# Kernel optimization log

Measured on AMD Instinct MI355X. Metric: run time of the kernel, lower is better.

## Reference

```python
import jax, jax.numpy as jnp
import numpy as np

P = 16  # patch size
D = 768  # embedding dim


def setup_inputs() -> dict:
    key = jax.random.key(0)
    k_img, k_w, k_b = jax.random.split(key, 3)
    B, H, W, C = 64, 224, 224, 3
    image = jax.random.normal(k_img, (B, H, W, C), dtype=jnp.float32)
    patch_dim = P * P * C  # 768
    # Keras Dense default: glorot_uniform kernel, zeros bias
    limit = np.sqrt(6.0 / (patch_dim + D)).astype(np.float32)
    W_proj = jax.random.uniform(k_w, (patch_dim, D), dtype=jnp.float32,
                                minval=-limit, maxval=limit)
    b_proj = jnp.zeros((D,), dtype=jnp.float32)
    return {"image": image, "W_proj": W_proj, "b_proj": b_proj}


def reference(image, W_proj, b_proj):
    B, H, W, C = image.shape
    nh, nw = H // P, W // P
    # Fused im2col replacing the per-patch slicing loop:
    # [B,H,W,C] -> [B, nh, P, nw, P, C] -> [B, nh, nw, P, P, C] -> [B, nh*nw, P*P*C]
    # Row-major (p_i, p_j) patch order matches the original nested loop, and
    # flatten of a [B,P,P,C] slice matches the (P,P,C) raveling here.
    patches = image.reshape(B, nh, P, nw, P, C)
    patches = patches.transpose(0, 1, 3, 2, 4, 5).reshape(B, nh * nw, P * P * C)
    # Dense + exact GELU (tf.keras.activations.gelu default approximate=False)
    x = jnp.einsum('bnp,pd->bnd', patches, W_proj) + b_proj
    return jax.nn.gelu(x, approximate=False)
```

## Files before the change

### kernel.cpp

```cpp
#include <hip/hip_runtime.h>
#include <hip/hip_bf16.h>
#include <math.h>

#define MM 12544
#define KK 768
#define NN 768
#define BM 64
#define BN 256
#define NKS 24
#define MT 196
#define NT 3
#define N64 12

#define A2_BLOCKS (MT * 4)
#define W_BLOCKS (N64 * NKS)
#define FRAG_BYTES 1024
#define KSTRIDE (4 * FRAG_BYTES)
#define PANEL_BYTES (NKS * KSTRIDE)

typedef __bf16 v8bf __attribute__((ext_vector_type(8)));
typedef float  v4f  __attribute__((ext_vector_type(4)));

__global__ __launch_bounds__(256) void pack_kernel(const float* __restrict__ img,
                                                   const float* __restrict__ w,
                                                   __hip_bfloat16* __restrict__ apack,
                                                   __hip_bfloat16* __restrict__ wpack) {
    const int tid = threadIdx.x;

    if (blockIdx.x < A2_BLOCKS) {
        const int blk = blockIdx.x;
        const int mt  = blk >> 2;
        const int c   = blk & 3;
        const int r   = tid & 63;
        const int il  = tid >> 6;
        const int i   = c * 4 + il;
        const int m   = mt * 64 + r;
        const int b   = m / 196;
        const int pm  = m - b * 196;
        const int pr  = pm / 14;
        const int pc  = pm - pr * 14;
        const float* src = img + (size_t)(((b * 224 + pr * 16 + i) * 224 + pc * 16) * 3);
        float4 f[12];
#pragma unroll
        for (int ld = 0; ld < 12; ld++) f[ld] = ((const float4*)src)[ld];

        const int fi   = r >> 4;
        const int l_lo = r & 15;
        uint4* dst = (uint4*)apack + ((size_t)(mt * 24) * 4 + fi) * 64 + l_lo;
#pragma unroll
        for (int j = 0; j < 6; j++) {
            const int G  = i * 6 + j;
            const int ks = G >> 2;
            const int lh = G & 3;
            union { __hip_bfloat16 hh[8]; uint4 uu; } o;
            o.hh[0] = __float2bfloat16(f[2*j].x);   o.hh[1] = __float2bfloat16(f[2*j].y);
            o.hh[2] = __float2bfloat16(f[2*j].z);   o.hh[3] = __float2bfloat16(f[2*j].w);
            o.hh[4] = __float2bfloat16(f[2*j+1].x); o.hh[5] = __float2bfloat16(f[2*j+1].y);
            o.hh[6] = __float2bfloat16(f[2*j+1].z); o.hh[7] = __float2bfloat16(f[2*j+1].w);
            dst[(size_t)ks * 256 + lh * 16] = o.uu;
        }
    } else {
        const int bid = blockIdx.x - A2_BLOCKS;
        const int gid = bid * 256 + tid;
        const int l    = gid & 63;
        const int fi   = (gid >> 6) & 3;
        const int wb   = gid >> 8;
        const int n64  = wb / NKS;
        const int ks   = wb - n64 * NKS;
        const int col  = n64 * 64 + fi * 16 + (l & 15);
        const int k0   = ks * 32 + (l >> 4) * 8;
        union { __hip_bfloat16 hh[8]; uint4 uu; } o;
#pragma unroll
        for (int j = 0; j < 8; j++) o.hh[j] = __float2bfloat16(w[(size_t)(k0 + j) * NN + col]);
        ((uint4*)wpack)[(size_t)((n64 * NKS + ks) * 4 + fi) * 64 + l] = o.uu;
    }
}

__device__ __forceinline__ float gelu_fast(float x) {
    float t2 = 1.5957691216057308f * x * (1.0f + 0.044715f * x * x);
    float e  = __expf(t2);
    float r  = __builtin_amdgcn_rcpf(e + 1.0f);
    return x - x * r;
}

__global__ __launch_bounds__(256, 3) void gemm_reg(const __hip_bfloat16* __restrict__ apack,
                                                   const __hip_bfloat16* __restrict__ wpack,
                                                   const float* __restrict__ bias,
                                                   float* __restrict__ out) {
    const int h   = blockIdx.x;
    const int xcd = h & 7;
    const int jj  = h >> 3;
    const int u   = (xcd < 4 ? xcd * 74 : 296 + (xcd - 4) * 73) + jj;
    const int nt  = u % 3;
    const int mt  = u / 3;

    const int tid  = threadIdx.x;
    const int lane = tid & 63;
    const int wave = tid >> 6;
    const int col  = lane & 15;
    const int quad = lane >> 4;

    const char* pA = (const char*)apack + (size_t)mt * PANEL_BYTES + lane * 16;
    const char* pB = (const char*)wpack + (size_t)(nt * 4 + wave) * PANEL_BYTES + lane * 16;

    v4f acc[4][4];
    const v4f vzero = {0.f, 0.f, 0.f, 0.f};
#pragma unroll
    for (int a = 0; a < 4; a++)
#pragma unroll
        for (int c = 0; c < 4; c++) acc[a][c] = vzero;

    v8bf aR[2][4], bR[2][4];
#pragma unroll
    for (int mi = 0; mi < 4; mi++) {
        aR[0][mi] = *(const v8bf*)(pA + mi * FRAG_BYTES);
        aR[1][mi] = *(const v8bf*)(pA + KSTRIDE + mi * FRAG_BYTES);
    }
#pragma unroll
    for (int ni = 0; ni < 4; ni++) {
        bR[0][ni] = *(const v8bf*)(pB + ni * FRAG_BYTES);
        bR[1][ni] = *(const v8bf*)(pB + KSTRIDE + ni * FRAG_BYTES);
    }

#pragma unroll
    for (int ks = 0; ks < NKS; ks++) {
        const int cur = ks & 1;
        __builtin_amdgcn_s_setprio(1);
#pragma unroll
        for (int mi = 0; mi < 4; mi++)
#pragma unroll
            for (int ni = 0; ni < 4; ni++)
                acc[mi][ni] = __builtin_amdgcn_mfma_f32_16x16x32_bf16(
                    aR[cur][mi], bR[cur][ni], acc[mi][ni], 0, 0, 0);
        __builtin_amdgcn_s_setprio(0);
        if (ks + 2 < NKS) {
            const char* qA = pA + (size_t)(ks + 2) * KSTRIDE;
            const char* qB = pB + (size_t)(ks + 2) * KSTRIDE;
#pragma unroll
            for (int mi = 0; mi < 4; mi++)
                aR[cur][mi] = *(const v8bf*)(qA + mi * FRAG_BYTES);
#pragma unroll
            for (int ni = 0; ni < 4; ni++)
                bR[cur][ni] = *(const v8bf*)(qB + ni * FRAG_BYTES);
        }
    }

#pragma unroll
    for (int ni = 0; ni < 4; ni++) {
        int n    = nt * BN + wave * 64 + ni * 16 + col;
        float bv = bias[n];
#pragma unroll
        for (int mi = 0; mi < 4; mi++) {
            int rowb = mt * BM + mi * 16 + quad * 4;
            float* po = out + (size_t)rowb * NN + n;
#pragma unroll
            for (int rg = 0; rg < 4; rg++) {
                float x = acc[mi][ni][rg] + bv;
                po[(size_t)rg * NN] = gelu_fast(x);
            }
        }
    }
}

extern "C" void kernel_launch(void* const* d_in, const int* in_sizes, int n_in,
                              void* d_out, int out_size, void* d_ws, size_t ws_size,
                              hipStream_t stream) {
    const float* img   = (const float*)d_in[0];
    const float* wproj = (const float*)d_in[1];
    const float* bias  = (const float*)d_in[2];
    float* out = (float*)d_out;

    __hip_bfloat16* apack = (__hip_bfloat16*)d_ws;
    __hip_bfloat16* wpack = (__hip_bfloat16*)((char*)d_ws + (size_t)MM * KK * 2);

    pack_kernel<<<dim3(A2_BLOCKS + W_BLOCKS), dim3(256), 0, stream>>>(
        img, wproj, apack, wpack);
    gemm_reg<<<dim3(MT * NT), dim3(256), 0, stream>>>(apack, wpack, bias, out);
}
```

Measured before the change: 120.5 us.

## Fuse pack and GEMM into one persistent kernel with atomic work queue

Replaces the separate pack and GEMM launches with a single persistent kernel of 768 blocks. Blocks pull items from an atomic queue: weight packing first, then image packing, then GEMM tiles. Each GEMM tile spin-waits on completion counters for the weight pack and for its own A panel. This removes the gap between the two launches and lets GEMM work overlap with packing, at the cost of a memset, atomic traffic and spin-wait stalls, plus a deadlock risk if ordering assumptions fail.

```diff
diff --git a/kernel.cpp b/kernel.cpp
--- a/kernel.cpp
+++ b/kernel.cpp
@@ -12,69 +12,23 @@
 #define NT 3
 #define N64 12
 
-#define A2_BLOCKS (MT * 4)
-#define W_BLOCKS (N64 * NKS)
+#define W_ITEMS 288
+#define A_ITEMS (MT * 4)
+#define PACK_ITEMS (W_ITEMS + A_ITEMS)
+#define G_ITEMS (MT * NT)
+#define TOTAL_ITEMS (PACK_ITEMS + G_ITEMS)
+#define NBLK_PERS 768
+
 #define FRAG_BYTES 1024
 #define KSTRIDE (4 * FRAG_BYTES)
 #define PANEL_BYTES (NKS * KSTRIDE)
 
+#define APACK_BYTES ((size_t)MM * KK * 2)
+#define WPACK_BYTES ((size_t)NN * KK * 2)
+#define CTRS_OFF (APACK_BYTES + WPACK_BYTES)
+
 typedef __bf16 v8bf __attribute__((ext_vector_type(8)));
 typedef float  v4f  __attribute__((ext_vector_type(4)));
-
-__global__ __launch_bounds__(256) void pack_kernel(const float* __restrict__ img,
-                                                   const float* __restrict__ w,
-                                                   __hip_bfloat16* __restrict__ apack,
-                                                   __hip_bfloat16* __restrict__ wpack) {
-    const int tid = threadIdx.x;
-
-    if (blockIdx.x < A2_BLOCKS) {
-        const int blk = blockIdx.x;
-        const int mt  = blk >> 2;
-        const int c   = blk & 3;
-        const int r   = tid & 63;
-        const int il  = tid >> 6;
-        const int i   = c * 4 + il;
-        const int m   = mt * 64 + r;
-        const int b   = m / 196;
-        const int pm  = m - b * 196;
-        const int pr  = pm / 14;
-        const int pc  = pm - pr * 14;
-        const float* src = img + (size_t)(((b * 224 + pr * 16 + i) * 224 + pc * 16) * 3);
-        float4 f[12];
-#pragma unroll
-        for (int ld = 0; ld < 12; ld++) f[ld] = ((const float4*)src)[ld];
-
-        const int fi   = r >> 4;
-        const int l_lo = r & 15;
-        uint4* dst = (uint4*)apack + ((size_t)(mt * 24) * 4 + fi) * 64 + l_lo;
-#pragma unroll
-        for (int j = 0; j < 6; j++) {
-            const int G  = i * 6 + j;
-            const int ks = G >> 2;
-            const int lh = G & 3;
-            union { __hip_bfloat16 hh[8]; uint4 uu; } o;
-            o.hh[0] = __float2bfloat16(f[2*j].x);   o.hh[1] = __float2bfloat16(f[2*j].y);
-            o.hh[2] = __float2bfloat16(f[2*j].z);   o.hh[3] = __float2bfloat16(f[2*j].w);
-            o.hh[4] = __float2bfloat16(f[2*j+1].x); o.hh[5] = __float2bfloat16(f[2*j+1].y);
-            o.hh[6] = __float2bfloat16(f[2*j+1].z); o.hh[7] = __float2bfloat16(f[2*j+1].w);
-            dst[(size_t)ks * 256 + lh * 16] = o.uu;
-        }
-    } else {
-        const int bid = blockIdx.x - A2_BLOCKS;
-        const int gid = bid * 256 + tid;
-        const int l    = gid & 63;
-        const int fi   = (gid >> 6) & 3;
-        const int wb   = gid >> 8;
-        const int n64  = wb / NKS;
-        const int ks   = wb - n64 * NKS;
-        const int col  = n64 * 64 + fi * 16 + (l & 15);
-        const int k0   = ks * 32 + (l >> 4) * 8;
-        union { __hip_bfloat16 hh[8]; uint4 uu; } o;
-#pragma unroll
-        for (int j = 0; j < 8; j++) o.hh[j] = __float2bfloat16(w[(size_t)(k0 + j) * NN + col]);
-        ((uint4*)wpack)[(size_t)((n64 * NKS + ks) * 4 + fi) * 64 + l] = o.uu;
-    }
-}
 
 __device__ __forceinline__ float gelu_fast(float x) {
     float t2 = 1.5957691216057308f * x * (1.0f + 0.044715f * x * x);
@@ -83,82 +37,161 @@
     return x - x * r;
 }
 
-__global__ __launch_bounds__(256, 3) void gemm_reg(const __hip_bfloat16* __restrict__ apack,
-                                                   const __hip_bfloat16* __restrict__ wpack,
-                                                   const float* __restrict__ bias,
-                                                   float* __restrict__ out) {
-    const int h   = blockIdx.x;
-    const int xcd = h & 7;
-    const int jj  = h >> 3;
-    const int u   = (xcd < 4 ? xcd * 74 : 296 + (xcd - 4) * 73) + jj;
-    const int nt  = u % 3;
-    const int mt  = u / 3;
-
-    const int tid  = threadIdx.x;
-    const int lane = tid & 63;
-    const int wave = tid >> 6;
-    const int col  = lane & 15;
-    const int quad = lane >> 4;
-
-    const char* pA = (const char*)apack + (size_t)mt * PANEL_BYTES + lane * 16;
-    const char* pB = (const char*)wpack + (size_t)(nt * 4 + wave) * PANEL_BYTES + lane * 16;
-
-    v4f acc[4][4];
-    const v4f vzero = {0.f, 0.f, 0.f, 0.f};
-#pragma unroll
-    for (int a = 0; a < 4; a++)
-#pragma unroll
-        for (int c = 0; c < 4; c++) acc[a][c] = vzero;
-
-    v8bf aR[2][4], bR[2][4];
-#pragma unroll
-    for (int mi = 0; mi < 4; mi++) {
-        aR[0][mi] = *(const v8bf*)(pA + mi * FRAG_BYTES);
-        aR[1][mi] = *(const v8bf*)(pA + KSTRIDE + mi * FRAG_BYTES);
-    }
-#pragma unroll
-    for (int ni = 0; ni < 4; ni++) {
-        bR[0][ni] = *(const v8bf*)(pB + ni * FRAG_BYTES);
-        bR[1][ni] = *(const v8bf*)(pB + KSTRIDE + ni * FRAG_BYTES);
-    }
-
-#pragma unroll
-    for (int ks = 0; ks < NKS; ks++) {
-        const int cur = ks & 1;
-        __builtin_amdgcn_s_setprio(1);
-#pragma unroll
-        for (int mi = 0; mi < 4; mi++)
-#pragma unroll
-            for (int ni = 0; ni < 4; ni++)
-                acc[mi][ni] = __builtin_amdgcn_mfma_f32_16x16x32_bf16(
-                    aR[cur][mi], bR[cur][ni], acc[mi][ni], 0, 0, 0);
-        __builtin_amdgcn_s_setprio(0);
-        if (ks + 2 < NKS) {
-            const char* qA = pA + (size_t)(ks + 2) * KSTRIDE;
-            const char* qB = pB + (size_t)(ks + 2) * KSTRIDE;
-#pragma unroll
-            for (int mi = 0; mi < 4; mi++)
-                aR[cur][mi] = *(const v8bf*)(qA + mi * FRAG_BYTES);
-#pragma unroll
-            for (int ni = 0; ni < 4; ni++)
-                bR[cur][ni] = *(const v8bf*)(qB + ni * FRAG_BYTES);
+__global__ __launch_bounds__(256, 3) void fused_all(const float* __restrict__ img,
+                                                    const float* __restrict__ w,
+                                                    const float* __restrict__ bias,
+                                                    float* __restrict__ out,
+                                                    __hip_bfloat16* __restrict__ apack,
+                                                    __hip_bfloat16* __restrict__ wpack,
+                                                    unsigned int* __restrict__ ctrs) {
+    unsigned int* queue = ctrs;
+    unsigned int* wdone = ctrs + 1;
+    unsigned int* adone = ctrs + 2;
+
+    __shared__ int s_item;
+    const int tid = threadIdx.x;
+
+    int it = blockIdx.x;
+    for (;;) {
+        if (it >= TOTAL_ITEMS) break;
+        unsigned int* fptr = nullptr;
+
+        if (it < W_ITEMS) {
+            const int l   = tid & 63;
+            const int fi  = tid >> 6;
+            const int n64 = it / NKS;
+            const int ks  = it - n64 * NKS;
+            const int col = n64 * 64 + fi * 16 + (l & 15);
+            const int k0  = ks * 32 + (l >> 4) * 8;
+            union { __hip_bfloat16 hh[8]; uint4 uu; } o;
+#pragma unroll
+            for (int j = 0; j < 8; j++)
+                o.hh[j] = __float2bfloat16(w[(size_t)(k0 + j) * NN + col]);
+            ((uint4*)wpack)[(size_t)((n64 * NKS + ks) * 4 + fi) * 64 + l] = o.uu;
+            fptr = wdone;
+        } else if (it < PACK_ITEMS) {
+            const int a   = it - W_ITEMS;
+            const int mt  = a >> 2;
+            const int c   = a & 3;
+            const int r   = tid & 63;
+            const int il  = tid >> 6;
+            const int i   = c * 4 + il;
+            const int m   = mt * 64 + r;
+            const int b   = m / 196;
+            const int pm  = m - b * 196;
+            const int pr  = pm / 14;
+            const int pc  = pm - pr * 14;
+            const float* src = img + (size_t)(((b * 224 + pr * 16 + i) * 224 + pc * 16) * 3);
+            float4 f[12];
+#pragma unroll
+            for (int ld = 0; ld < 12; ld++) f[ld] = ((const float4*)src)[ld];
+            const int fi   = r >> 4;
+            const int l_lo = r & 15;
+            uint4* dst = (uint4*)apack + ((size_t)(mt * 24) * 4 + fi) * 64 + l_lo;
+#pragma unroll
+            for (int j = 0; j < 6; j++) {
+                const int G  = i * 6 + j;
+                const int ks = G >> 2;
+                const int lh = G & 3;
+                union { __hip_bfloat16 hh[8]; uint4 uu; } o;
+                o.hh[0] = __float2bfloat16(f[2*j].x);   o.hh[1] = __float2bfloat16(f[2*j].y);
+                o.hh[2] = __float2bfloat16(f[2*j].z);   o.hh[3] = __float2bfloat16(f[2*j].w);
+                o.hh[4] = __float2bfloat16(f[2*j+1].x); o.hh[5] = __float2bfloat16(f[2*j+1].y);
+                o.hh[6] = __float2bfloat16(f[2*j+1].z); o.hh[7] = __float2bfloat16(f[2*j+1].w);
+                dst[(size_t)ks * 256 + lh * 16] = o.uu;
+            }
+            fptr = &adone[mt];
+        } else {
+            const int g  = it - PACK_ITEMS;
+            const int mt = g / 3;
+            const int nt = g - mt * 3;
+
+            if (tid == 0) {
+                while (__hip_atomic_load(wdone, __ATOMIC_RELAXED,
+                                         __HIP_MEMORY_SCOPE_AGENT) < W_ITEMS)
+                    __builtin_amdgcn_s_sleep(2);
+                while (__hip_atomic_load(&adone[mt], __ATOMIC_RELAXED,
+                                         __HIP_MEMORY_SCOPE_AGENT) < 4)
+                    __builtin_amdgcn_s_sleep(2);
+            }
+            __syncthreads();
+            __threadfence();
+
+            const int lane = tid & 63;
+            const int wave = tid >> 6;
+            const int col  = lane & 15;
+            const int quad = lane >> 4;
+
+            const char* pA = (const char*)apack + (size_t)mt * PANEL_BYTES + lane * 16;
+            const char* pB = (const char*)wpack + (size_t)(nt * 4 + wave) * PANEL_BYTES + lane * 16;
+
+            v4f acc[4][4];
+            const v4f vzero = {0.f, 0.f, 0.f, 0.f};
+#pragma unroll
+            for (int aa = 0; aa < 4; aa++)
+#pragma unroll
+                for (int cc = 0; cc < 4; cc++) acc[aa][cc] = vzero;
+
+            v8bf aR[2][4], bR[2][4];
+#pragma unroll
+            for (int mi = 0; mi < 4; mi++) {
+                aR[0][mi] = *(const v8bf*)(pA + mi * FRAG_BYTES);
+                aR[1][mi] = *(const v8bf*)(pA + KSTRIDE + mi * FRAG_BYTES);
+            }
+#pragma unroll
+            for (int ni = 0; ni < 4; ni++) {
+                bR[0][ni] = *(const v8bf*)(pB + ni * FRAG_BYTES);
+                bR[1][ni] = *(const v8bf*)(pB + KSTRIDE + ni * FRAG_BYTES);
+            }
+#pragma unroll
+            for (int ks = 0; ks < NKS; ks++) {
+                const int cur = ks & 1;
+                __builtin_amdgcn_s_setprio(1);
+#pragma unroll
+                for (int mi = 0; mi < 4; mi++)
+#pragma unroll
+                    for (int ni = 0; ni < 4; ni++)
+                        acc[mi][ni] = __builtin_amdgcn_mfma_f32_16x16x32_bf16(
+                            aR[cur][mi], bR[cur][ni], acc[mi][ni], 0, 0, 0);
+                __builtin_amdgcn_s_setprio(0);
+                if (ks + 2 < NKS) {
+                    const char* qA = pA + (size_t)(ks + 2) * KSTRIDE;
+                    const char* qB = pB + (size_t)(ks + 2) * KSTRIDE;
+#pragma unroll
+                    for (int mi = 0; mi < 4; mi++)
+                        aR[cur][mi] = *(const v8bf*)(qA + mi * FRAG_BYTES);
+#pragma unroll
+                    for (int ni = 0; ni < 4; ni++)
+                        bR[cur][ni] = *(const v8bf*)(qB + ni * FRAG_BYTES);
+                }
+            }
+#pragma unroll
+            for (int ni = 0; ni < 4; ni++) {
+                int n    = nt * BN + wave * 64 + ni * 16 + col;
+                float bv = bias[n];
+#pragma unroll
+                for (int mi = 0; mi < 4; mi++) {
+                    int rowb = mt * BM + mi * 16 + quad * 4;
+                    float* po = out + (size_t)rowb * NN + n;
+#pragma unroll
+                    for (int rg = 0; rg < 4; rg++) {
+                        float x = acc[mi][ni][rg] + bv;
+                        po[(size_t)rg * NN] = gelu_fast(x);
+                    }
+                }
+            }
         }
-    }
-
-#pragma unroll
-    for (int ni = 0; ni < 4; ni++) {
-        int n    = nt * BN + wave * 64 + ni * 16 + col;
-        float bv = bias[n];
-#pragma unroll
-        for (int mi = 0; mi < 4; mi++) {
-            int rowb = mt * BM + mi * 16 + quad * 4;
-            float* po = out + (size_t)rowb * NN + n;
-#pragma unroll
-            for (int rg = 0; rg < 4; rg++) {
-                float x = acc[mi][ni][rg] + bv;
-                po[(size_t)rg * NN] = gelu_fast(x);
-            }
+
+        __syncthreads();
+        if (tid == 0) {
+            if (fptr) {
+                __threadfence();
+                atomicAdd(fptr, 1u);
+            }
+            s_item = NBLK_PERS + (int)atomicAdd(queue, 1u);
         }
+        __syncthreads();
+        it = s_item;
     }
 }
 
@@ -171,9 +204,10 @@
     float* out = (float*)d_out;
 
     __hip_bfloat16* apack = (__hip_bfloat16*)d_ws;
-    __hip_bfloat16* wpack = (__hip_bfloat16*)((char*)d_ws + (size_t)MM * KK * 2);
-
-    pack_kernel<<<dim3(A2_BLOCKS + W_BLOCKS), dim3(256), 0, stream>>>(
-        img, wproj, apack, wpack);
-    gemm_reg<<<dim3(MT * NT), dim3(256), 0, stream>>>(apack, wpack, bias, out);
+    __hip_bfloat16* wpack = (__hip_bfloat16*)((char*)d_ws + APACK_BYTES);
+    unsigned int*   ctrs  = (unsigned int*)((char*)d_ws + CTRS_OFF);
+
+    hipMemsetAsync(ctrs, 0, 1024, stream);
+    fused_all<<<dim3(NBLK_PERS), dim3(256), 0, stream>>>(
+        img, wproj, bias, out, apack, wpack, ctrs);
 }
```

Measured after the change: 245.0 us. +103.3%, slower.
